# Performance work log

Hardware: AMD Instinct MI355X
Metric: run time of the kernel (lower is better)

Reference implementation:

```python
import jax, jax.numpy as jnp
import numpy as np

N = 100000      # nodes
NE = 1250000    # edges
D = 64          # in_dim == out_dim
H = 8           # heads
DH = D // H     # per-head dim


def setup_inputs() -> dict:
    key = jax.random.key(0)
    ks = jax.random.split(key, 7)
    s = 1.0 / np.sqrt(D)
    return {
        "x": jax.random.normal(ks[0], (N, D), jnp.float32),
        "edge_attr": jax.random.normal(ks[1], (NE, D), jnp.float32),
        "WQ": jax.random.normal(ks[2], (D, D), jnp.float32) * s,
        "WK": jax.random.normal(ks[3], (D, D), jnp.float32) * s,
        "WV": jax.random.normal(ks[4], (D, D), jnp.float32) * s,
        "WE": jax.random.normal(ks[5], (D, D), jnp.float32) * s,
        "edge_index": jax.random.randint(ks[6], (2, NE), 0, N, dtype=jnp.int32),
    }


def reference(x, edge_attr, WQ, WK, WV, WE, edge_index):
    # Linear projections (torch Linear y = x W^T; here W is stored [in,out])
    Q = (x @ WQ).reshape(N, H, DH)
    K = (x @ WK).reshape(N, H, DH)
    V = (x @ WV).reshape(N, H, DH)
    Ef = (edge_attr @ WE).reshape(NE, H, DH)

    src = edge_index[0]
    dst = edge_index[1]

    # per-edge score: exp(clamp(sum_d K[src]*Q[dst]*E / sqrt(DH), -5, 5))
    score = (K[src] * Q[dst]) * (1.0 / np.sqrt(DH)) * Ef  # [E,H,DH]
    score = jnp.exp(jnp.clip(score.sum(-1, keepdims=True), -5.0, 5.0))  # [E,H,1]

    msg = V[src] * score  # [E,H,DH]
    wV = jax.ops.segment_sum(msg, dst, num_segments=N)    # [N,H,DH]
    Z = jax.ops.segment_sum(score, dst, num_segments=N)   # [N,H,1]

    h_out = wV / (Z + 1e-6)
    return h_out.reshape(N, H * DH)
```

## Files before the change

### kernel.cpp

```cpp
#include <hip/hip_runtime.h>
#include <hip/hip_bf16.h>

#define NN    100000
#define NEDGE 1250000

typedef __attribute__((ext_vector_type(8))) short bf16x8;
typedef __attribute__((ext_vector_type(8))) unsigned short u16x8;
typedef __attribute__((ext_vector_type(4))) float f32x4;

__device__ __forceinline__ short f2bf(float f) {
    unsigned u = __float_as_uint(f);
    u += 0x7FFFu + ((u >> 16) & 1u);
    return (short)(u >> 16);
}
__device__ __forceinline__ float bf2f(unsigned short u) {
    return __uint_as_float(((unsigned)u) << 16);
}

constexpr size_t OFF_Q    = 0;
constexpr size_t OFF_KB   = OFF_Q    + (size_t)NN * 64 * 4;
constexpr size_t OFF_VB   = OFF_KB   + (size_t)NN * 64 * 2;
constexpr size_t OFF_EFS  = OFF_VB   + (size_t)NN * 64 * 2;
constexpr size_t OFF_SSRC = OFF_EFS  + (size_t)NEDGE * 64 * 2;
constexpr size_t OFF_POSE = OFF_SSRC + (size_t)NEDGE * 4;
constexpr size_t OFF_HIST = OFF_POSE + (size_t)NEDGE * 4;
constexpr size_t OFF_EX   = OFF_HIST + (size_t)NN * 4;
constexpr size_t OFF_BSUM = OFF_EX   + (size_t)NN * 4;
constexpr size_t OFF_BOFF = OFF_BSUM + 512 * 4;
constexpr size_t OFF_START= OFF_BOFF + 512 * 4;
constexpr size_t OFF_CUR  = OFF_START+ (size_t)(NN + 1) * 4;
constexpr size_t WS_NEED  = OFF_CUR  + (size_t)NN * 4;
constexpr int NB_SCAN = (NN + 255) / 256;

__global__ __launch_bounds__(256) void qkv_kernel(
    const float* __restrict__ x,
    const float* __restrict__ WQ, const float* __restrict__ WK,
    const float* __restrict__ WV,
    float* __restrict__ Qf, unsigned short* __restrict__ Kb,
    unsigned short* __restrict__ Vb)
{
    const int lane = threadIdx.x & 63;
    const int wid  = threadIdx.x >> 6;
    const int gw   = blockIdx.x * 4 + wid;
    const int nw   = gridDim.x * 4;
    const int colb = lane & 15;
    const int krow = (lane >> 4) * 8;

    bf16x8 Bf[3][4][2];
    const float* Ws[3] = {WQ, WK, WV};
    #pragma unroll
    for (int m = 0; m < 3; ++m)
        #pragma unroll
        for (int n = 0; n < 4; ++n)
            #pragma unroll
            for (int kh = 0; kh < 2; ++kh) {
                bf16x8 b;
                #pragma unroll
                for (int j = 0; j < 8; ++j)
                    b[j] = f2bf(Ws[m][(size_t)(kh * 32 + krow + j) * 64 + n * 16 + colb]);
                Bf[m][n][kh] = b;
            }

    for (int tile = gw; tile < NN / 16; tile += nw) {
        const int r0 = tile * 16;
        const float* xr = x + (size_t)(r0 + colb) * 64 + krow;
        f32x4 a0 = *(const f32x4*)(xr);
        f32x4 a1 = *(const f32x4*)(xr + 4);
        f32x4 a2 = *(const f32x4*)(xr + 32);
        f32x4 a3 = *(const f32x4*)(xr + 36);
        bf16x8 Alo, Ahi;
        #pragma unroll
        for (int j = 0; j < 4; ++j) {
            Alo[j]     = f2bf(a0[j]);
            Alo[4 + j] = f2bf(a1[j]);
            Ahi[j]     = f2bf(a2[j]);
            Ahi[4 + j] = f2bf(a3[j]);
        }
        #pragma unroll
        for (int m = 0; m < 3; ++m) {
            #pragma unroll
            for (int n = 0; n < 4; ++n) {
                f32x4 acc = {0.f, 0.f, 0.f, 0.f};
                acc = __builtin_amdgcn_mfma_f32_16x16x32_bf16(Alo, Bf[m][n][0], acc, 0, 0, 0);
                acc = __builtin_amdgcn_mfma_f32_16x16x32_bf16(Ahi, Bf[m][n][1], acc, 0, 0, 0);
                #pragma unroll
                for (int q = 0; q < 4; ++q) {
                    const size_t idx = (size_t)(r0 + (lane >> 4) * 4 + q) * 64 + n * 16 + colb;
                    if (m == 0)      Qf[idx] = acc[q];
                    else if (m == 1) Kb[idx] = (unsigned short)f2bf(acc[q]);
                    else             Vb[idx] = (unsigned short)f2bf(acc[q]);
                }
            }
        }
    }
}

__global__ void zero_hist_kernel(int* __restrict__ hist) {
    const int i = blockIdx.x * blockDim.x + threadIdx.x;
    if (i < NN) hist[i] = 0;
}

__global__ void hist_kernel(const int* __restrict__ ei, int* __restrict__ hist) {
    const int e = blockIdx.x * blockDim.x + threadIdx.x;
    if (e < NEDGE) atomicAdd(&hist[ei[NEDGE + e]], 1);
}

__global__ __launch_bounds__(256) void scanA_kernel(
    const int* __restrict__ hist, int* __restrict__ ex, int* __restrict__ bsum)
{
    __shared__ int wsum[4];
    const int i = blockIdx.x * 256 + threadIdx.x;
    const int lane = threadIdx.x & 63, wid = threadIdx.x >> 6;
    const int v = (i < NN) ? hist[i] : 0;
    int incl = v;
    #pragma unroll
    for (int off = 1; off < 64; off <<= 1) {
        int t = __shfl_up(incl, off);
        if (lane >= off) incl += t;
    }
    if (lane == 63) wsum[wid] = incl;
    __syncthreads();
    int pre = 0, bt = 0;
    #pragma unroll
    for (int w = 0; w < 4; ++w) { int s = wsum[w]; bt += s; if (w < wid) pre += s; }
    if (i < NN) ex[i] = incl - v + pre;
    if (threadIdx.x == 0) bsum[blockIdx.x] = bt;
}

__global__ __launch_bounds__(512) void scanB_kernel(
    const int* __restrict__ bsum, int* __restrict__ boff)
{
    __shared__ int wsum[8];
    const int i = threadIdx.x;
    const int lane = i & 63, wid = i >> 6;
    const int v = (i < NB_SCAN) ? bsum[i] : 0;
    int incl = v;
    #pragma unroll
    for (int off = 1; off < 64; off <<= 1) {
        int t = __shfl_up(incl, off);
        if (lane >= off) incl += t;
    }
    if (lane == 63) wsum[wid] = incl;
    __syncthreads();
    int pre = 0;
    #pragma unroll
    for (int w = 0; w < 8; ++w) { if (w < wid) pre += wsum[w]; }
    if (i < NB_SCAN) boff[i] = incl - v + pre;
}

__global__ void scanC_kernel(const int* __restrict__ ex, const int* __restrict__ boff,
                             int* __restrict__ start, int* __restrict__ cursor)
{
    const int i = blockIdx.x * blockDim.x + threadIdx.x;
    if (i < NN) {
        const int s = ex[i] + boff[i >> 8];
        start[i] = s;
        cursor[i] = s;
    } else if (i == NN) {
        start[NN] = NEDGE;
    }
}

__global__ void scatter_kernel(const int* __restrict__ ei, int* __restrict__ cursor,
                               int* __restrict__ ssrc, int* __restrict__ pose)
{
    const int e = blockIdx.x * blockDim.x + threadIdx.x;
    if (e < NEDGE) {
        const int dst = ei[NEDGE + e];
        const int pos = atomicAdd(&cursor[dst], 1);
        ssrc[pos] = ei[e];
        pose[e] = pos;
    }
}

__global__ __launch_bounds__(256) void ef_kernel(
    const float* __restrict__ edge_attr, const float* __restrict__ WE,
    const int* __restrict__ pose, unsigned short* __restrict__ Efs)
{
    const int lane = threadIdx.x & 63;
    const int wid  = threadIdx.x >> 6;
    const int gw   = blockIdx.x * 4 + wid;
    const int nw   = gridDim.x * 4;
    const int colb = lane & 15;
    const int krow = (lane >> 4) * 8;

    bf16x8 Bf[4][2];
    #pragma unroll
    for (int n = 0; n < 4; ++n)
        #pragma unroll
        for (int kh = 0; kh < 2; ++kh) {
            bf16x8 b;
            #pragma unroll
            for (int j = 0; j < 8; ++j)
                b[j] = f2bf(WE[(size_t)(kh * 32 + krow + j) * 64 + n * 16 + colb]);
            Bf[n][kh] = b;
        }

    for (int tile = gw; tile < NEDGE / 16; tile += nw) {
        const int e0 = tile * 16;
        const float* ear = edge_attr + (size_t)(e0 + colb) * 64 + krow;
        f32x4 a0 = *(const f32x4*)(ear);
        f32x4 a1 = *(const f32x4*)(ear + 4);
        f32x4 a2 = *(const f32x4*)(ear + 32);
        f32x4 a3 = *(const f32x4*)(ear + 36);
        bf16x8 Alo, Ahi;
        #pragma unroll
        for (int j = 0; j < 4; ++j) {
            Alo[j]     = f2bf(a0[j]);
            Alo[4 + j] = f2bf(a1[j]);
            Ahi[j]     = f2bf(a2[j]);
            Ahi[4 + j] = f2bf(a3[j]);
        }
        int posq[4];
        #pragma unroll
        for (int q = 0; q < 4; ++q)
            posq[q] = pose[e0 + (lane >> 4) * 4 + q];
        #pragma unroll
        for (int n = 0; n < 4; ++n) {
            f32x4 z = {0.f, 0.f, 0.f, 0.f};
            z = __builtin_amdgcn_mfma_f32_16x16x32_bf16(Alo, Bf[n][0], z, 0, 0, 0);
            z = __builtin_amdgcn_mfma_f32_16x16x32_bf16(Ahi, Bf[n][1], z, 0, 0, 0);
            #pragma unroll
            for (int q = 0; q < 4; ++q)
                Efs[(size_t)posq[q] * 64 + n * 16 + colb] = (unsigned short)f2bf(z[q]);
        }
    }
}

__global__ __launch_bounds__(256) void agg_kernel(
    const float* __restrict__ Qn, const unsigned short* __restrict__ Kb,
    const unsigned short* __restrict__ Vb, const unsigned short* __restrict__ Efs,
    const int* __restrict__ start, const int* __restrict__ ssrc,
    float* __restrict__ out)
{
    const int lane = threadIdx.x & 63;
    const int gw = (blockIdx.x * blockDim.x + threadIdx.x) >> 6;
    const int nw = (gridDim.x * blockDim.x) >> 6;
    const int el = lane >> 3;
    const int h  = lane & 7;
    const float c = 0.35355339059327373f;

    for (int dst = gw; dst < NN; dst += nw) {
        const int beg = start[dst], end = start[dst + 1];
        const float* qp = Qn + (size_t)dst * 64 + h * 8;
        const f32x4 q0 = *(const f32x4*)(qp);
        const f32x4 q1 = *(const f32x4*)(qp + 4);
        f32x4 av0 = {0.f, 0.f, 0.f, 0.f};
        f32x4 av1 = {0.f, 0.f, 0.f, 0.f};
        float az = 0.f;

        for (int j = beg; j < end; j += 16) {
            const int jeA = j + el;
            const int jeB = j + el + 8;
            const bool aA = jeA < end;
            const bool aB = jeB < end;
            const int iA = aA ? jeA : beg;
            const int iB = aB ? jeB : beg;
            const int sA = ssrc[iA];
            const int sB = ssrc[iB];
            const u16x8 kA = *(const u16x8*)(Kb  + (size_t)sA * 64 + h * 8);
            const u16x8 vA = *(const u16x8*)(Vb  + (size_t)sA * 64 + h * 8);
            const u16x8 eA = *(const u16x8*)(Efs + (size_t)iA * 64 + h * 8);
            const u16x8 kB = *(const u16x8*)(Kb  + (size_t)sB * 64 + h * 8);
            const u16x8 vB = *(const u16x8*)(Vb  + (size_t)sB * 64 + h * 8);
            const u16x8 eB = *(const u16x8*)(Efs + (size_t)iB * 64 + h * 8);

            float tA = 0.f, tB = 0.f;
            #pragma unroll
            for (int d = 0; d < 4; ++d) {
                tA += bf2f(kA[d])     * q0[d] * bf2f(eA[d]);
                tA += bf2f(kA[4 + d]) * q1[d] * bf2f(eA[4 + d]);
                tB += bf2f(kB[d])     * q0[d] * bf2f(eB[d]);
                tB += bf2f(kB[4 + d]) * q1[d] * bf2f(eB[4 + d]);
            }
            const float scA = aA ? __expf(fminf(fmaxf(tA * c, -5.f), 5.f)) : 0.f;
            const float scB = aB ? __expf(fminf(fmaxf(tB * c, -5.f), 5.f)) : 0.f;
            az += scA + scB;
            #pragma unroll
            for (int d = 0; d < 4; ++d) {
                av0[d] += bf2f(vA[d])     * scA + bf2f(vB[d])     * scB;
                av1[d] += bf2f(vA[4 + d]) * scA + bf2f(vB[4 + d]) * scB;
            }
        }

        #pragma unroll
        for (int off = 8; off < 64; off <<= 1) {
            az += __shfl_xor(az, off);
            #pragma unroll
            for (int d = 0; d < 4; ++d) {
                av0[d] += __shfl_xor(av0[d], off);
                av1[d] += __shfl_xor(av1[d], off);
            }
        }

        if (el == 0) {
            const float inv = 1.f / (az + 1e-6f);
            f32x4 o0, o1;
            #pragma unroll
            for (int d = 0; d < 4; ++d) { o0[d] = av0[d] * inv; o1[d] = av1[d] * inv; }
            float* op = out + (size_t)dst * 64 + h * 8;
            *(f32x4*)(op)     = o0;
            *(f32x4*)(op + 4) = o1;
        }
    }
}

__global__ __launch_bounds__(256) void edge_kernel_fb(
    const float* __restrict__ edge_attr, const float* __restrict__ WE,
    const float* __restrict__ Qn, const unsigned short* __restrict__ Kb,
    const unsigned short* __restrict__ Vb, const int* __restrict__ ei,
    float* __restrict__ outAcc, float* __restrict__ Z)
{
    const int lane = threadIdx.x & 63;
    const int wid  = threadIdx.x >> 6;
    const int gw   = blockIdx.x * 4 + wid;
    const int nw   = gridDim.x * 4;
    const int colb = lane & 15;
    const int krow = (lane >> 4) * 8;
    const int b8   = (lane >> 3) & 1;

    bf16x8 Bf[4][2];
    #pragma unroll
    for (int n = 0; n < 4; ++n)
        #pragma unroll
        for (int kh = 0; kh < 2; ++kh) {
            bf16x8 b;
            #pragma unroll
            for (int j = 0; j < 8; ++j)
                b[j] = f2bf(WE[(size_t)(kh * 32 + krow + j) * 64 + n * 16 + colb]);
            Bf[n][kh] = b;
        }

    const float inv_sqrt_dh = 0.35355339059327373f;

    for (int tile = gw; tile < NEDGE / 16; tile += nw) {
        const int e0 = tile * 16;
        const float* ear = edge_attr + (size_t)(e0 + colb) * 64 + krow;
        f32x4 a0 = *(const f32x4*)(ear);
        f32x4 a1 = *(const f32x4*)(ear + 4);
        f32x4 a2 = *(const f32x4*)(ear + 32);
        f32x4 a3 = *(const f32x4*)(ear + 36);
        bf16x8 Alo, Ahi;
        #pragma unroll
        for (int j = 0; j < 4; ++j) {
            Alo[j]     = f2bf(a0[j]);
            Alo[4 + j] = f2bf(a1[j]);
            Ahi[j]     = f2bf(a2[j]);
            Ahi[4 + j] = f2bf(a3[j]);
        }
        f32x4 acc[4];
        #pragma unroll
        for (int n = 0; n < 4; ++n) {
            f32x4 z = {0.f, 0.f, 0.f, 0.f};
            z = __builtin_amdgcn_mfma_f32_16x16x32_bf16(Alo, Bf[n][0], z, 0, 0, 0);
            z = __builtin_amdgcn_mfma_f32_16x16x32_bf16(Ahi, Bf[n][1], z, 0, 0, 0);
            acc[n] = z;
        }
        int srcq[4], dstq[4];
        #pragma unroll
        for (int q = 0; q < 4; ++q) {
            const int erl = (lane >> 4) * 4 + q;
            srcq[q] = ei[e0 + erl];
            dstq[q] = ei[NEDGE + e0 + erl];
        }
        float sc[4][4];
        #pragma unroll
        for (int q = 0; q < 4; ++q) {
            #pragma unroll
            for (int n = 0; n < 4; ++n) {
                const int cidx = n * 16 + colb;
                const float kv = bf2f(Kb[(size_t)srcq[q] * 64 + cidx]);
                const float qv = Qn[(size_t)dstq[q] * 64 + cidx];
                float t = kv * qv * acc[n][q];
                t += __shfl_xor(t, 1);
                t += __shfl_xor(t, 2);
                t += __shfl_xor(t, 4);
                const float s = fminf(fmaxf(t * inv_sqrt_dh, -5.0f), 5.0f);
                sc[q][n] = __expf(s);
            }
        }
        #pragma unroll
        for (int q = 0; q < 4; ++q) {
            #pragma unroll
            for (int n = 0; n < 4; ++n) {
                const int cidx = n * 16 + colb;
                const float vv = bf2f(Vb[(size_t)srcq[q] * 64 + cidx]);
                unsafeAtomicAdd(&outAcc[(size_t)dstq[q] * 64 + cidx], vv * sc[q][n]);
                if ((lane & 7) == 0) {
                    const int hh = 2 * n + b8;
                    unsafeAtomicAdd(&Z[(size_t)dstq[q] * 8 + hh], sc[q][n]);
                }
            }
        }
    }
}

__global__ void finalize_fb(float* __restrict__ out, const float* __restrict__ Z) {
    const int i = blockIdx.x * blockDim.x + threadIdx.x;
    if (i < NN * 64) {
        const int node = i >> 6;
        const int h    = (i >> 3) & 7;
        out[i] = out[i] / (Z[node * 8 + h] + 1e-6f);
    }
}

extern "C" void kernel_launch(void* const* d_in, const int* in_sizes, int n_in,
                              void* d_out, int out_size, void* d_ws, size_t ws_size,
                              hipStream_t stream) {
    const float* x         = (const float*)d_in[0];
    const float* edge_attr = (const float*)d_in[1];
    const float* WQ        = (const float*)d_in[2];
    const float* WK        = (const float*)d_in[3];
    const float* WV        = (const float*)d_in[4];
    const float* WE        = (const float*)d_in[5];
    const int*   ei        = (const int*)d_in[6];
    float* out = (float*)d_out;

    char* base = (char*)d_ws;
    float*          Qf = (float*)(base + OFF_Q);
    unsigned short* Kb = (unsigned short*)(base + OFF_KB);
    unsigned short* Vb = (unsigned short*)(base + OFF_VB);

    qkv_kernel<<<1563, 256, 0, stream>>>(x, WQ, WK, WV, Qf, Kb, Vb);

    if (ws_size >= WS_NEED) {
        unsigned short* Efs = (unsigned short*)(base + OFF_EFS);
        int* ssrc   = (int*)(base + OFF_SSRC);
        int* pose   = (int*)(base + OFF_POSE);
        int* hist   = (int*)(base + OFF_HIST);
        int* ex     = (int*)(base + OFF_EX);
        int* bsum   = (int*)(base + OFF_BSUM);
        int* boff   = (int*)(base + OFF_BOFF);
        int* start  = (int*)(base + OFF_START);
        int* cursor = (int*)(base + OFF_CUR);

        zero_hist_kernel<<<NB_SCAN, 256, 0, stream>>>(hist);
        hist_kernel<<<(NEDGE + 255) / 256, 256, 0, stream>>>(ei, hist);
        scanA_kernel<<<NB_SCAN, 256, 0, stream>>>(hist, ex, bsum);
        scanB_kernel<<<1, 512, 0, stream>>>(bsum, boff);
        scanC_kernel<<<(NN + 256) / 256 + 1, 256, 0, stream>>>(ex, boff, start, cursor);
        scatter_kernel<<<(NEDGE + 255) / 256, 256, 0, stream>>>(ei, cursor, ssrc, pose);
        ef_kernel<<<4096, 256, 0, stream>>>(edge_attr, WE, pose, Efs);
        agg_kernel<<<4096, 256, 0, stream>>>(Qf, Kb, Vb, Efs, start, ssrc, out);
    } else {
        float* Z = (float*)(base + OFF_EFS);
        hipMemsetAsync(d_out, 0, (size_t)NN * 64 * sizeof(float), stream);
        hipMemsetAsync(Z, 0, (size_t)NN * 8 * sizeof(float), stream);
        edge_kernel_fb<<<2048, 256, 0, stream>>>(edge_attr, WE, Qf, Kb, Vb, ei, out, Z);
        finalize_fb<<<(NN * 64 + 255) / 256, 256, 0, stream>>>(out, Z);
    }
}
```

Before: 384.9 us.

## Fuse edge projection into destination-sorted aggregation kernel via per-wave LDS staging

Removes the separate ef_kernel and the bf16 Efs intermediate buffer. The scatter now writes (src, edge id) pairs, and the aggregation kernel computes each 16-edge tile's edge_attr@WE projection with MFMA, staging it in per-wave LDS before scoring. This avoids writing and re-reading 160MB of Efs and one launch. In exchange it reads edge_attr rows in gather order rather than sequentially, pays MFMA cost for padded partial tiles of low-degree nodes, and adds a zero-degree early exit.

After: 345.1 us. -10.3%, faster.

```diff
diff --git a/kernel.cpp b/kernel.cpp
--- a/kernel.cpp
+++ b/kernel.cpp
@@ -20,10 +20,8 @@
 constexpr size_t OFF_Q    = 0;
 constexpr size_t OFF_KB   = OFF_Q    + (size_t)NN * 64 * 4;
 constexpr size_t OFF_VB   = OFF_KB   + (size_t)NN * 64 * 2;
-constexpr size_t OFF_EFS  = OFF_VB   + (size_t)NN * 64 * 2;
-constexpr size_t OFF_SSRC = OFF_EFS  + (size_t)NEDGE * 64 * 2;
-constexpr size_t OFF_POSE = OFF_SSRC + (size_t)NEDGE * 4;
-constexpr size_t OFF_HIST = OFF_POSE + (size_t)NEDGE * 4;
+constexpr size_t OFF_SRT  = OFF_VB   + (size_t)NN * 64 * 2;
+constexpr size_t OFF_HIST = OFF_SRT  + (size_t)NEDGE * 8;
 constexpr size_t OFF_EX   = OFF_HIST + (size_t)NN * 4;
 constexpr size_t OFF_BSUM = OFF_EX   + (size_t)NN * 4;
 constexpr size_t OFF_BOFF = OFF_BSUM + 512 * 4;
@@ -162,27 +160,37 @@
 }
 
 __global__ void scatter_kernel(const int* __restrict__ ei, int* __restrict__ cursor,
-                               int* __restrict__ ssrc, int* __restrict__ pose)
+                               int2* __restrict__ sorted)
 {
     const int e = blockIdx.x * blockDim.x + threadIdx.x;
     if (e < NEDGE) {
         const int dst = ei[NEDGE + e];
         const int pos = atomicAdd(&cursor[dst], 1);
-        ssrc[pos] = ei[e];
-        pose[e] = pos;
-    }
-}
-
-__global__ __launch_bounds__(256) void ef_kernel(
+        sorted[pos] = make_int2(ei[e], e);
+    }
+}
+
+__global__ __launch_bounds__(256) void agg_kernel(
+    const float* __restrict__ Qn, const unsigned short* __restrict__ Kb,
+    const unsigned short* __restrict__ Vb,
     const float* __restrict__ edge_attr, const float* __restrict__ WE,
-    const int* __restrict__ pose, unsigned short* __restrict__ Efs)
+    const int* __restrict__ start, const int2* __restrict__ sorted,
+    float* __restrict__ out)
 {
     const int lane = threadIdx.x & 63;
     const int wid  = threadIdx.x >> 6;
-    const int gw   = blockIdx.x * 4 + wid;
-    const int nw   = gridDim.x * 4;
+    const int gw   = (blockIdx.x * blockDim.x + threadIdx.x) >> 6;
+    const int nw   = (gridDim.x * blockDim.x) >> 6;
     const int colb = lane & 15;
     const int krow = (lane >> 4) * 8;
+    const int el   = lane >> 3;
+    const int h    = lane & 7;
+    const float c  = 0.35355339059327373f;
+
+    __shared__ float efs_all[4][16][68];
+    __shared__ int   srcs_all[4][16];
+    float (*efs)[68] = efs_all[wid];
+    int*   srcs      = srcs_all[wid];
 
     bf16x8 Bf[4][2];
     #pragma unroll
@@ -196,52 +204,17 @@
             Bf[n][kh] = b;
         }
 
-    for (int tile = gw; tile < NEDGE / 16; tile += nw) {
-        const int e0 = tile * 16;
-        const float* ear = edge_attr + (size_t)(e0 + colb) * 64 + krow;
-        f32x4 a0 = *(const f32x4*)(ear);
-        f32x4 a1 = *(const f32x4*)(ear + 4);
-        f32x4 a2 = *(const f32x4*)(ear + 32);
-        f32x4 a3 = *(const f32x4*)(ear + 36);
-        bf16x8 Alo, Ahi;
-        #pragma unroll
-        for (int j = 0; j < 4; ++j) {
-            Alo[j]     = f2bf(a0[j]);
-            Alo[4 + j] = f2bf(a1[j]);
-            Ahi[j]     = f2bf(a2[j]);
-            Ahi[4 + j] = f2bf(a3[j]);
-        }
-        int posq[4];
-        #pragma unroll
-        for (int q = 0; q < 4; ++q)
-            posq[q] = pose[e0 + (lane >> 4) * 4 + q];
-        #pragma unroll
-        for (int n = 0; n < 4; ++n) {
-            f32x4 z = {0.f, 0.f, 0.f, 0.f};
-            z = __builtin_amdgcn_mfma_f32_16x16x32_bf16(Alo, Bf[n][0], z, 0, 0, 0);
-            z = __builtin_amdgcn_mfma_f32_16x16x32_bf16(Ahi, Bf[n][1], z, 0, 0, 0);
-            #pragma unroll
-            for (int q = 0; q < 4; ++q)
-                Efs[(size_t)posq[q] * 64 + n * 16 + colb] = (unsigned short)f2bf(z[q]);
-        }
-    }
-}
-
-__global__ __launch_bounds__(256) void agg_kernel(
-    const float* __restrict__ Qn, const unsigned short* __restrict__ Kb,
-    const unsigned short* __restrict__ Vb, const unsigned short* __restrict__ Efs,
-    const int* __restrict__ start, const int* __restrict__ ssrc,
-    float* __restrict__ out)
-{
-    const int lane = threadIdx.x & 63;
-    const int gw = (blockIdx.x * blockDim.x + threadIdx.x) >> 6;
-    const int nw = (gridDim.x * blockDim.x) >> 6;
-    const int el = lane >> 3;
-    const int h  = lane & 7;
-    const float c = 0.35355339059327373f;
-
     for (int dst = gw; dst < NN; dst += nw) {
         const int beg = start[dst], end = start[dst + 1];
+        if (beg == end) {
+            if (el == 0) {
+                float* op = out + (size_t)dst * 64 + h * 8;
+                const f32x4 zz = {0.f, 0.f, 0.f, 0.f};
+                *(f32x4*)(op)     = zz;
+                *(f32x4*)(op + 4) = zz;
+            }
+            continue;
+        }
         const float* qp = Qn + (size_t)dst * 64 + h * 8;
         const f32x4 q0 = *(const f32x4*)(qp);
         const f32x4 q1 = *(const f32x4*)(qp + 4);
@@ -250,36 +223,58 @@
         float az = 0.f;
 
         for (int j = beg; j < end; j += 16) {
-            const int jeA = j + el;
-            const int jeB = j + el + 8;
-            const bool aA = jeA < end;
-            const bool aB = jeB < end;
-            const int iA = aA ? jeA : beg;
-            const int iB = aB ? jeB : beg;
-            const int sA = ssrc[iA];
-            const int sB = ssrc[iB];
-            const u16x8 kA = *(const u16x8*)(Kb  + (size_t)sA * 64 + h * 8);
-            const u16x8 vA = *(const u16x8*)(Vb  + (size_t)sA * 64 + h * 8);
-            const u16x8 eA = *(const u16x8*)(Efs + (size_t)iA * 64 + h * 8);
-            const u16x8 kB = *(const u16x8*)(Kb  + (size_t)sB * 64 + h * 8);
-            const u16x8 vB = *(const u16x8*)(Vb  + (size_t)sB * 64 + h * 8);
-            const u16x8 eB = *(const u16x8*)(Efs + (size_t)iB * 64 + h * 8);
-
-            float tA = 0.f, tB = 0.f;
-            #pragma unroll
-            for (int d = 0; d < 4; ++d) {
-                tA += bf2f(kA[d])     * q0[d] * bf2f(eA[d]);
-                tA += bf2f(kA[4 + d]) * q1[d] * bf2f(eA[4 + d]);
-                tB += bf2f(kB[d])     * q0[d] * bf2f(eB[d]);
-                tB += bf2f(kB[4 + d]) * q1[d] * bf2f(eB[4 + d]);
-            }
-            const float scA = aA ? __expf(fminf(fmaxf(tA * c, -5.f), 5.f)) : 0.f;
-            const float scB = aB ? __expf(fminf(fmaxf(tB * c, -5.f), 5.f)) : 0.f;
-            az += scA + scB;
-            #pragma unroll
-            for (int d = 0; d < 4; ++d) {
-                av0[d] += bf2f(vA[d])     * scA + bf2f(vB[d])     * scB;
-                av1[d] += bf2f(vA[4 + d]) * scA + bf2f(vB[4 + d]) * scB;
+            int rpos = j + colb;
+            if (rpos >= end) rpos = beg;
+            const int2 se = sorted[rpos];
+            if (lane < 16) srcs[lane] = se.x;
+            const float* ear = edge_attr + (size_t)se.y * 64 + krow;
+            f32x4 a0 = *(const f32x4*)(ear);
+            f32x4 a1 = *(const f32x4*)(ear + 4);
+            f32x4 a2 = *(const f32x4*)(ear + 32);
+            f32x4 a3 = *(const f32x4*)(ear + 36);
+            bf16x8 Alo, Ahi;
+            #pragma unroll
+            for (int jj = 0; jj < 4; ++jj) {
+                Alo[jj]     = f2bf(a0[jj]);
+                Alo[4 + jj] = f2bf(a1[jj]);
+                Ahi[jj]     = f2bf(a2[jj]);
+                Ahi[4 + jj] = f2bf(a3[jj]);
+            }
+            const int rbase = (lane >> 4) * 4;
+            #pragma unroll
+            for (int n = 0; n < 4; ++n) {
+                f32x4 z = {0.f, 0.f, 0.f, 0.f};
+                z = __builtin_amdgcn_mfma_f32_16x16x32_bf16(Alo, Bf[n][0], z, 0, 0, 0);
+                z = __builtin_amdgcn_mfma_f32_16x16x32_bf16(Ahi, Bf[n][1], z, 0, 0, 0);
+                #pragma unroll
+                for (int q = 0; q < 4; ++q)
+                    efs[rbase + q][n * 16 + colb] = z[q];
+            }
+            asm volatile("s_waitcnt lgkmcnt(0)" ::: "memory");
+            __builtin_amdgcn_sched_barrier(0);
+
+            #pragma unroll
+            for (int t = 0; t < 2; ++t) {
+                const int er  = el + t * 8;
+                const bool act = (j + er) < end;
+                const int srcT = srcs[er];
+                const u16x8 kT = *(const u16x8*)(Kb + (size_t)srcT * 64 + h * 8);
+                const u16x8 vT = *(const u16x8*)(Vb + (size_t)srcT * 64 + h * 8);
+                const f32x4 e0 = *(const f32x4*)(&efs[er][h * 8]);
+                const f32x4 e1 = *(const f32x4*)(&efs[er][h * 8 + 4]);
+                float tt = 0.f;
+                #pragma unroll
+                for (int d = 0; d < 4; ++d) {
+                    tt += bf2f(kT[d])     * q0[d] * e0[d];
+                    tt += bf2f(kT[4 + d]) * q1[d] * e1[d];
+                }
+                const float sc = act ? __expf(fminf(fmaxf(tt * c, -5.f), 5.f)) : 0.f;
+                az += sc;
+                #pragma unroll
+                for (int d = 0; d < 4; ++d) {
+                    av0[d] += bf2f(vT[d])     * sc;
+                    av1[d] += bf2f(vT[4 + d]) * sc;
+                }
             }
         }
 
@@ -424,26 +419,23 @@
     qkv_kernel<<<1563, 256, 0, stream>>>(x, WQ, WK, WV, Qf, Kb, Vb);
 
     if (ws_size >= WS_NEED) {
-        unsigned short* Efs = (unsigned short*)(base + OFF_EFS);
-        int* ssrc   = (int*)(base + OFF_SSRC);
-        int* pose   = (int*)(base + OFF_POSE);
-        int* hist   = (int*)(base + OFF_HIST);
-        int* ex     = (int*)(base + OFF_EX);
-        int* bsum   = (int*)(base + OFF_BSUM);
-        int* boff   = (int*)(base + OFF_BOFF);
-        int* start  = (int*)(base + OFF_START);
-        int* cursor = (int*)(base + OFF_CUR);
+        int2* sorted = (int2*)(base + OFF_SRT);
+        int* hist    = (int*)(base + OFF_HIST);
+        int* ex      = (int*)(base + OFF_EX);
+        int* bsum    = (int*)(base + OFF_BSUM);
+        int* boff    = (int*)(base + OFF_BOFF);
+        int* start   = (int*)(base + OFF_START);
+        int* cursor  = (int*)(base + OFF_CUR);
 
         zero_hist_kernel<<<NB_SCAN, 256, 0, stream>>>(hist);
         hist_kernel<<<(NEDGE + 255) / 256, 256, 0, stream>>>(ei, hist);
         scanA_kernel<<<NB_SCAN, 256, 0, stream>>>(hist, ex, bsum);
         scanB_kernel<<<1, 512, 0, stream>>>(bsum, boff);
         scanC_kernel<<<(NN + 256) / 256 + 1, 256, 0, stream>>>(ex, boff, start, cursor);
-        scatter_kernel<<<(NEDGE + 255) / 256, 256, 0, stream>>>(ei, cursor, ssrc, pose);
-        ef_kernel<<<4096, 256, 0, stream>>>(edge_attr, WE, pose, Efs);
-        agg_kernel<<<4096, 256, 0, stream>>>(Qf, Kb, Vb, Efs, start, ssrc, out);
+        scatter_kernel<<<(NEDGE + 255) / 256, 256, 0, stream>>>(ei, cursor, sorted);
+        agg_kernel<<<4096, 256, 0, stream>>>(Qf, Kb, Vb, edge_attr, WE, start, sorted, out);
     } else {
-        float* Z = (float*)(base + OFF_EFS);
+        float* Z = (float*)(base + OFF_SRT);
         hipMemsetAsync(d_out, 0, (size_t)NN * 64 * sizeof(float), stream);
         hipMemsetAsync(Z, 0, (size_t)NN * 8 * sizeof(float), stream);
         edge_kernel_fb<<<2048, 256, 0, stream>>>(edge_attr, WE, Qf, Kb, Vb, ei, out, Z);
```
